# Performance work log

Measured on AMD Instinct MI355X. Metric: run time of the kernel, lower is better.

The kernel has to match this reference:

```python
import jax, jax.numpy as jnp
import numpy as np

B, H, S, DK, DV = 2, 16, 2048, 64, 64

def setup_inputs() -> dict:
    key = jax.random.key(0)
    kq, kk, kv, km = jax.random.split(key, 4)
    q = jax.random.normal(kq, (B, H, S, DK), dtype=jnp.float32)
    k = jax.random.normal(kk, (B, H, S, DK), dtype=jnp.float32)
    v = jax.random.normal(kv, (B, H, S, DV), dtype=jnp.float32)
    mask = jax.random.randint(km, (B, H, S, S), 0, 2).astype(jnp.bool_)
    return {"q": q, "k": k, "v": v, "mask": mask}

def reference(q, k, v, mask):
    d_k = q.shape[-1]
    # scores: [B, H, Sq, Sk]
    scores = jnp.einsum('bhqd,bhkd->bhqk', q, k) / np.sqrt(d_k).astype(jnp.float32)
    scores = jnp.where(mask, jnp.float32(-1e9), scores)
    attn = jax.nn.softmax(scores, axis=-1)
    return jnp.einsum('bhqk,bhkd->bhqd', attn, v)
```

## Files before the change

### kernel.cpp

```cpp
#include <hip/hip_runtime.h>


#define LOG2E 1.4426950408889634f
#define QSCALE (0.125f * LOG2E)

typedef __attribute__((ext_vector_type(8))) short short8;
typedef __attribute__((ext_vector_type(4))) short short4v;
typedef __attribute__((ext_vector_type(4))) float f32x4;
typedef unsigned __attribute__((ext_vector_type(4))) uintv4;

constexpr int S = 2048, D = 64;

__device__ __forceinline__ short bf16rne(float x) {
  union { float f; unsigned u; } cv; cv.f = x;
  unsigned u = cv.u;
  u += 0x7fffu + ((u >> 16) & 1u);
  return (short)(u >> 16);
}

__device__ __forceinline__ void glds16(const void* g, void* l) {
  __builtin_amdgcn_global_load_lds(
      (const __attribute__((address_space(1))) void*)g,
      (__attribute__((address_space(3))) void*)l, 16, 0, 0);
}

__global__ void prep(const float* __restrict__ kp, const float* __restrict__ vp,
                     short* __restrict__ kb, short* __restrict__ vt,
                     const unsigned* __restrict__ m, int* __restrict__ flag) {
  const int b = blockIdx.x;
  const int tid = threadIdx.x;
  if (b == 0 && tid < 64) {
    unsigned v = m[tid];
    unsigned long long big = __ballot(v > 1u && v != 0x3F800000u);
    unsigned long long isf = __ballot(v == 0x3F800000u);
    if (tid == 0) *flag = (big != 0ull && isf == 0ull) ? 1 : 0;
  }
  if (b < 2048) {
    size_t i = ((size_t)b * 256 + tid) * 8;
    float4 a = *(const float4*)(kp + i);
    float4 c = *(const float4*)(kp + i + 4);
    short8 s;
    s[0] = bf16rne(a.x); s[1] = bf16rne(a.y); s[2] = bf16rne(a.z); s[3] = bf16rne(a.w);
    s[4] = bf16rne(c.x); s[5] = bf16rne(c.y); s[6] = bf16rne(c.z); s[7] = bf16rne(c.w);
    *(short8*)&kb[i] = s;
  } else {
    __shared__ float tile[64][65];
    const int bb = b - 2048;
    const int bh = bb >> 5, k0 = (bb & 31) * 64;
    const float* src = vp + ((size_t)(bh * S + k0)) * D;
#pragma unroll
    for (int i = 0; i < 4; ++i) {
      int row = i * 16 + (tid >> 4);
      int col = (tid & 15) * 4;
      float4 x = *(const float4*)(src + row * D + col);
      tile[row][col] = x.x; tile[row][col + 1] = x.y;
      tile[row][col + 2] = x.z; tile[row][col + 3] = x.w;
    }
    __syncthreads();
#pragma unroll
    for (int i = 0; i < 4; ++i) {
      int dim = i * 16 + (tid >> 4);
      int kb4 = (tid & 15) * 4;
      short4v s;
#pragma unroll
      for (int j = 0; j < 4; ++j) s[j] = bf16rne(tile[kb4 + j][dim]);
      *(short4v*)&vt[((size_t)(bh * D + dim)) * S + k0 + kb4] = s;
    }
  }
}

__launch_bounds__(256, 4)
__global__ void attn_fwd(const float* __restrict__ qp, const short* __restrict__ kb,
                         const short* __restrict__ vt, const void* __restrict__ mp,
                         float* __restrict__ op, const int* __restrict__ fmtp) {
  const int fmt  = *fmtp;
  const int tid  = threadIdx.x;
  const int lane = tid & 63;
  const int w    = tid >> 6;
  const int c    = lane & 15;
  const int quad = lane >> 4;

  const int bh = blockIdx.x >> 5;
  const int q0 = (blockIdx.x & 31) * 64;

  __shared__ short ks[2][64 * 64];
  __shared__ short vs[2][64 * 64];

  const float* qg = qp + ((size_t)(bh * S + q0 + w * 16 + c)) * D;
  short8 qB[2];
#pragma unroll
  for (int kk = 0; kk < 2; ++kk) {
    const float* p = qg + kk * 32 + quad * 8;
    float4 x = *(const float4*)(p);
    float4 y = *(const float4*)(p + 4);
    short8 f;
    f[0] = bf16rne(x.x * QSCALE); f[1] = bf16rne(x.y * QSCALE);
    f[2] = bf16rne(x.z * QSCALE); f[3] = bf16rne(x.w * QSCALE);
    f[4] = bf16rne(y.x * QSCALE); f[5] = bf16rne(y.y * QSCALE);
    f[6] = bf16rne(y.z * QSCALE); f[7] = bf16rne(y.w * QSCALE);
    qB[kk] = f;
  }

  f32x4 O[4];
#pragma unroll
  for (int t = 0; t < 4; ++t) O[t] = (f32x4){0.f, 0.f, 0.f, 0.f};
  f32x4 Lv = (f32x4){0.f, 0.f, 0.f, 0.f};

  const int rsub = lane >> 3;
  const int cswV = (lane & 7) ^ rsub;
  const int cswK = cswV ^ ((w & 1) << 2);
  const short* kbase = kb + ((size_t)(bh * S)) * D;
  const short* vbase = vt + ((size_t)(bh * D)) * S;

  const int sw0 = ((quad    ) ^ (c & 7)) * 8;
  const int sw1 = ((quad | 4) ^ (c & 7)) * 8;
  const int kx  = (((c >> 2) & 1) << 2);

  const size_t mrow = ((size_t)(bh * S + q0 + w * 16 + c)) * S;

  unsigned long long mm0, mm1;

  auto stage = [&](int it, int buf) {
    const int k0 = it * 64;
#pragma unroll
    for (int h2 = 0; h2 < 2; ++h2) {
      const int row = (h2 * 4 + w) * 8 + rsub;
      glds16(kbase + (size_t)(k0 + row) * 64 + cswK * 8,
             (char*)&ks[buf][0] + (h2 * 4 + w) * 1024);
      glds16(vbase + (size_t)row * S + k0 + cswV * 8,
             (char*)&vs[buf][0] + (h2 * 4 + w) * 1024);
    }
  };

  auto mload = [&](int it) {
    const int kO = it * 64;
    if (fmt == 1) {
      const unsigned char* mq = (const unsigned char*)mp + mrow + kO + 8 * quad;
      mm0 = __builtin_nontemporal_load((const unsigned long long*)mq);
      mm1 = __builtin_nontemporal_load((const unsigned long long*)(mq + 32));
    } else {
#pragma unroll
      for (int h = 0; h < 2; ++h) {
        const unsigned* m0 = (const unsigned*)mp + mrow + kO + h * 32 + 8 * quad;
        uintv4 a = __builtin_nontemporal_load((const uintv4*)m0);
        uintv4 b = __builtin_nontemporal_load((const uintv4*)(m0 + 4));
        unsigned long long t = 0ull;
#pragma unroll
        for (int j = 0; j < 4; ++j) {
          if (a[j]) t |= 0xffull << (8 * j);
          if (b[j]) t |= 0xffull << (8 * (j + 4));
        }
        if (h == 0) mm0 = t; else mm1 = t;
      }
    }
  };

  stage(0, 0);
  mload(0);

  for (int it = 0; it < 32; ++it) {
    const int buf = it & 1;
    __syncthreads();

    if (it + 1 < 32) stage(it + 1, buf ^ 1);

    const unsigned long long mb0 = mm0, mb1 = mm1;
    if (it + 1 < 32) mload(it + 1);

    __builtin_amdgcn_s_setprio(1);

    short8 pa0, pa1;
#pragma unroll
    for (int g = 0; g < 4; ++g) {
      const int r7 = (c & 3) + 4 * (g & 1);
      const int rr = ((g & 2) << 4) + 8 * (c >> 2) + r7;
      const int px = ((quad ^ r7 ^ kx)) * 8;
      short8 ka0 = *(const short8*)&ks[buf][rr * 64 + px];
      short8 ka1 = *(const short8*)&ks[buf][rr * 64 + (px ^ 32)];
      f32x4 z = (f32x4){0.f, 0.f, 0.f, 0.f};
      z = __builtin_amdgcn_mfma_f32_16x16x32_bf16(ka0, qB[0], z, 0, 0, 0);
      z = __builtin_amdgcn_mfma_f32_16x16x32_bf16(ka1, qB[1], z, 0, 0, 0);
      const unsigned long long mq64 = (g & 2) ? mb1 : mb0;
      const unsigned mw = (g & 1) ? (unsigned)(mq64 >> 32) : (unsigned)mq64;
#pragma unroll
      for (int r = 0; r < 4; ++r) {
        const int j = 4 * (g & 1) + r;
        float e = ((mw >> (8 * r)) & 0xffu) ? 0.f : exp2f(z[r]);
        Lv[r] += e;
        if (g & 2) pa1[j] = bf16rne(e); else pa0[j] = bf16rne(e);
      }
    }

#pragma unroll
    for (int t = 0; t < 4; ++t) {
      short8 vb0 = *(const short8*)&vs[buf][(16 * t + c) * 64 + sw0];
      short8 vb1 = *(const short8*)&vs[buf][(16 * t + c) * 64 + sw1];
      O[t] = __builtin_amdgcn_mfma_f32_16x16x32_bf16(pa0, vb0, O[t], 0, 0, 0);
      O[t] = __builtin_amdgcn_mfma_f32_16x16x32_bf16(pa1, vb1, O[t], 0, 0, 0);
    }

    __builtin_amdgcn_s_setprio(0);
  }

  float Lt = (Lv[0] + Lv[1]) + (Lv[2] + Lv[3]);
  Lt += __shfl_xor(Lt, 16);
  Lt += __shfl_xor(Lt, 32);
#pragma unroll
  for (int r = 0; r < 4; ++r) {
    float Lr = __shfl(Lt, (lane & 48) | (quad * 4 + r));
    float inv = 1.f / Lr;
    const size_t ob = ((size_t)(bh * S + q0 + w * 16 + quad * 4 + r)) * D;
#pragma unroll
    for (int t = 0; t < 4; ++t) op[ob + 16 * t + c] = O[t][r] * inv;
  }
}

extern "C" void kernel_launch(void* const* d_in, const int* in_sizes, int n_in,
                              void* d_out, int out_size, void* d_ws, size_t ws_size,
                              hipStream_t stream) {
  const float* q = (const float*)d_in[0];
  const float* k = (const float*)d_in[1];
  const float* v = (const float*)d_in[2];
  const void*  m = d_in[3];

  short* kbuf = (short*)d_ws;
  short* vtb  = (short*)((char*)d_ws + (8u << 20));
  int* flag   = (int*)((char*)d_ws + (16u << 20));

  prep<<<3072, 256, 0, stream>>>(k, v, kbuf, vtb, (const unsigned*)m, flag);
  attn_fwd<<<1024, 256, 0, stream>>>(q, kbuf, vtb, m, (float*)d_out, flag);
}
```

Measured before the change: 747.2 us.

## Prefetch mask two tiles ahead with explicit vmcnt waits and unrolled pipeline

Restructures the main loop into pairs of iterations with two register buffers for mask words, so mask loads are issued two K-tiles ahead instead of one. `__syncthreads` is replaced with explicit `s_waitcnt vmcnt(2)` plus `s_barrier`, so each iteration waits only for the K/V LDS stage and the older mask load, not for every outstanding load. The intent is to hide more of the latency of the large mask stream. It relies on hand-counted in-order vmcnt semantics, which becomes fragile if the number of loads per stage or per mask load changes (for example the fmt!=1 path).

```diff
diff --git a/kernel.cpp b/kernel.cpp
--- a/kernel.cpp
+++ b/kernel.cpp
@@ -118,7 +118,7 @@
 
   const size_t mrow = ((size_t)(bh * S + q0 + w * 16 + c)) * S;
 
-  unsigned long long mm0, mm1;
+  unsigned long long mmA0, mmA1, mmB0, mmB1;
 
   auto stage = [&](int it, int buf) {
     const int k0 = it * 64;
@@ -132,12 +132,12 @@
     }
   };
 
-  auto mload = [&](int it) {
+  auto mload = [&](unsigned long long& d0, unsigned long long& d1, int it) {
     const int kO = it * 64;
     if (fmt == 1) {
       const unsigned char* mq = (const unsigned char*)mp + mrow + kO + 8 * quad;
-      mm0 = __builtin_nontemporal_load((const unsigned long long*)mq);
-      mm1 = __builtin_nontemporal_load((const unsigned long long*)(mq + 32));
+      d0 = __builtin_nontemporal_load((const unsigned long long*)mq);
+      d1 = __builtin_nontemporal_load((const unsigned long long*)(mq + 32));
     } else {
 #pragma unroll
       for (int h = 0; h < 2; ++h) {
@@ -150,25 +150,13 @@
           if (a[j]) t |= 0xffull << (8 * j);
           if (b[j]) t |= 0xffull << (8 * (j + 4));
         }
-        if (h == 0) mm0 = t; else mm1 = t;
+        if (h == 0) d0 = t; else d1 = t;
       }
     }
   };
 
-  stage(0, 0);
-  mload(0);
-
-  for (int it = 0; it < 32; ++it) {
-    const int buf = it & 1;
-    __syncthreads();
-
-    if (it + 1 < 32) stage(it + 1, buf ^ 1);
-
-    const unsigned long long mb0 = mm0, mb1 = mm1;
-    if (it + 1 < 32) mload(it + 1);
-
+  auto compute = [&](int buf, unsigned long long mb0, unsigned long long mb1) {
     __builtin_amdgcn_s_setprio(1);
-
     short8 pa0, pa1;
 #pragma unroll
     for (int g = 0; g < 4; ++g) {
@@ -190,7 +178,6 @@
         if (g & 2) pa1[j] = bf16rne(e); else pa0[j] = bf16rne(e);
       }
     }
-
 #pragma unroll
     for (int t = 0; t < 4; ++t) {
       short8 vb0 = *(const short8*)&vs[buf][(16 * t + c) * 64 + sw0];
@@ -198,8 +185,48 @@
       O[t] = __builtin_amdgcn_mfma_f32_16x16x32_bf16(pa0, vb0, O[t], 0, 0, 0);
       O[t] = __builtin_amdgcn_mfma_f32_16x16x32_bf16(pa1, vb1, O[t], 0, 0, 0);
     }
-
     __builtin_amdgcn_s_setprio(0);
+  };
+
+  stage(0, 0);
+  asm volatile("" ::: "memory");
+  mload(mmA0, mmA1, 0);
+  mload(mmB0, mmB1, 1);
+
+#pragma unroll 1
+  for (int ip = 0; ip < 15; ++ip) {
+    const int itE = 2 * ip;
+    asm volatile("s_waitcnt vmcnt(2)" ::: "memory");
+    __builtin_amdgcn_s_barrier();
+    stage(itE + 1, 1);
+    asm volatile("" ::: "memory");
+    {
+      const unsigned long long b0 = mmA0, b1 = mmA1;
+      mload(mmA0, mmA1, itE + 2);
+      compute(0, b0, b1);
+    }
+    asm volatile("s_waitcnt vmcnt(2)" ::: "memory");
+    __builtin_amdgcn_s_barrier();
+    stage(itE + 2, 0);
+    asm volatile("" ::: "memory");
+    {
+      const unsigned long long b0 = mmB0, b1 = mmB1;
+      mload(mmB0, mmB1, itE + 3);
+      compute(1, b0, b1);
+    }
+  }
+  asm volatile("s_waitcnt vmcnt(2)" ::: "memory");
+  __builtin_amdgcn_s_barrier();
+  stage(31, 1);
+  {
+    const unsigned long long b0 = mmA0, b1 = mmA1;
+    compute(0, b0, b1);
+  }
+  asm volatile("s_waitcnt vmcnt(0)" ::: "memory");
+  __builtin_amdgcn_s_barrier();
+  {
+    const unsigned long long b0 = mmB0, b1 = mmB1;
+    compute(1, b0, b1);
   }
 
   float Lt = (Lv[0] + Lv[1]) + (Lv[2] + Lv[3]);
```

Measured after the change: 748.1 us. About the same (+0.1%).
